# Performance work log

Hardware: AMD Instinct MI355X
Metric: run time of the kernel (lower is better)

Reference implementation:

```python
import jax, jax.numpy as jnp
import numpy as np


def setup_inputs() -> dict:
    key = jax.random.key(0)
    k1, k2, k3, k4 = jax.random.split(key, 4)
    B1, N1, B2, N2, D = 64, 128, 64, 128, 128
    v1 = jax.random.normal(k1, (B1, N1, D), dtype=jnp.float32)
    v2 = jax.random.normal(k2, (B2, N2, D), dtype=jnp.float32)
    sz1 = jax.random.randint(k3, (B1,), 0, 128, dtype=jnp.int64)
    sz2 = jax.random.randint(k4, (B2,), 0, 128, dtype=jnp.int64)
    return {"v1": v1, "sz1": sz1, "v2": v2, "sz2": sz2}


def reference(v1, sz1, v2, sz2):
    # v1: (B1, N1, D) padded node features; v2: (B2, N2, D)
    # Pairwise Euclidean distances dist[b1,b2,i,j] = ||v1[b1,i] - v2[b2,j]||
    # via the gemm identity instead of the original's 5D broadcast.
    x2 = jnp.sum(v1 * v1, axis=-1)                     # (B1, N1)
    y2 = jnp.sum(v2 * v2, axis=-1)                     # (B2, N2)
    xy = jnp.einsum('aid,bjd->abij', v1, v2)           # (B1, B2, N1, N2)
    sq = x2[:, None, :, None] + y2[None, :, None, :] - 2.0 * xy
    dist = jnp.sqrt(jnp.maximum(sq, 0.0))              # (B1, B2, N1, N2)

    N1, N2 = v1.shape[1], v2.shape[1]
    mask1 = jnp.arange(N1)[None, :] >= sz1[:, None]    # (B1, N1) padded v1 nodes
    mask2 = jnp.arange(N2)[None, :] >= sz2[:, None]    # (B2, N2) padded v2 nodes
    mask = mask1[:, None, :, None] | mask2[None, :, None, :]  # (B1, B2, N1, N2)

    # Original fills masked entries with the global max of the (unmasked) distances.
    maximum = dist.max()
    dm = jnp.where(mask, maximum, dist)

    bm1 = dm.min(axis=2)                               # min over v1 nodes -> (B1, B2, N2)
    bm2 = dm.min(axis=3)                               # min over v2 nodes -> (B1, B2, N1)
    bm1 = jnp.where(jnp.all(mask, axis=2), 0.0, bm1)   # zero fully-masked columns
    bm2 = jnp.where(jnp.all(mask, axis=3), 0.0, bm2)   # zero fully-masked rows

    return bm1.sum(axis=2) + bm2.sum(axis=2)           # (B1, B2)
```

## Files before the change

### kernel.cpp

```cpp
#include <hip/hip_runtime.h>
#include <math.h>


typedef __attribute__((ext_vector_type(8))) short short8;
typedef __attribute__((ext_vector_type(4))) float f32x4;
typedef unsigned int u32;
typedef unsigned short ushort_t;

static __device__ __forceinline__ ushort_t f32_to_bf16_rne(float f) {
    u32 b = __float_as_uint(f);
    b += 0x7FFFu + ((b >> 16) & 1u);
    return (ushort_t)(b >> 16);
}

__global__ __launch_bounds__(256) void softhd_pre(
    const float* __restrict__ v1, const float* __restrict__ v2,
    ushort_t* __restrict__ v1b, ushort_t* __restrict__ v2b,
    float* __restrict__ x2g, float* __restrict__ y2g)
{
    int flat = blockIdx.x * 256 + threadIdx.x;
    int c = flat & 15;
    int r = (flat >> 4) & 127;
    int b = (flat >> 11) & 63;
    int t = flat >> 17;

    const float* src = (t ? v2 : v1) + ((size_t)((b << 7) + r) << 7) + c * 8;
    char* dstp = (char*)((t ? v2b : v1b) + ((size_t)b << 14));

    float4 q0 = *(const float4*)(src);
    float4 q1 = *(const float4*)(src + 4);

    ushort_t h[8];
    h[0] = f32_to_bf16_rne(q0.x); h[1] = f32_to_bf16_rne(q0.y);
    h[2] = f32_to_bf16_rne(q0.z); h[3] = f32_to_bf16_rne(q0.w);
    h[4] = f32_to_bf16_rne(q1.x); h[5] = f32_to_bf16_rne(q1.y);
    h[6] = f32_to_bf16_rne(q1.z); h[7] = f32_to_bf16_rne(q1.w);

    float p = 0.f;
#pragma unroll
    for (int k = 0; k < 8; ++k) {
        float fv = __uint_as_float((u32)h[k] << 16);
        p += fv * fv;
    }

    uint4 w;
    w.x = (u32)h[0] | ((u32)h[1] << 16);
    w.y = (u32)h[2] | ((u32)h[3] << 16);
    w.z = (u32)h[4] | ((u32)h[5] << 16);
    w.w = (u32)h[6] | ((u32)h[7] << 16);

    int off = ((c >> 2) << 13) + ((r >> 3) << 9) + ((c & 3) << 7) + ((r & 7) << 4);
    *(uint4*)(dstp + off) = w;

    p += __shfl_xor(p, 1);
    p += __shfl_xor(p, 2);
    p += __shfl_xor(p, 4);
    p += __shfl_xor(p, 8);
    if (c == 0) (t ? y2g : x2g)[(b << 7) + r] = p;
}

__global__ __launch_bounds__(256, 4) void softhd_mfma(
    const ushort_t* __restrict__ v1b, const ushort_t* __restrict__ v2b,
    const float* __restrict__ x2g, const float* __restrict__ y2g,
    const int* __restrict__ sz1, const int* __restrict__ sz2,
    float* __restrict__ out)
{
    __shared__ __align__(16) ushort_t sb[2][2][4096];
    __shared__ float sx2[128], sy2[128];
    __shared__ u32 sbm1[128], sbm2[128];
    __shared__ float swsum[4];

    const int tid = threadIdx.x;
    const int lane = tid & 63;
    const int wid = tid >> 6;
    const int bid = ((blockIdx.x & 7) << 9) | (blockIdx.x >> 3);
    const int b1 = bid >> 6, b2 = bid & 63;

    const char* gp0 = (const char*)(v1b + ((size_t)b1 << 14));
    const char* gp1 = (const char*)(v2b + ((size_t)b2 << 14));

    const int n1 = min(max(sz1[b1], 0), 128);
    const int n2 = min(max(sz2[b2], 0), 128);

    if (tid < 128) {
        sx2[tid] = x2g[(b1 << 7) + tid];
        sbm1[tid] = 0x7F800000u;
    } else {
        sy2[tid - 128] = y2g[(b2 << 7) + (tid - 128)];
        sbm2[tid - 128] = 0x7F800000u;
    }
    asm volatile("" ::: "memory");

#define STAGE(d, q)                                                          \
    {                                                                        \
        _Pragma("unroll")                                                    \
        for (int e = 0; e < 2; ++e) {                                        \
            int m16 = ((e << 8) + tid) << 4;                                 \
            __builtin_amdgcn_global_load_lds(                                \
                (const __attribute__((address_space(1))) u32*)(gp0 + ((q) << 13) + m16), \
                (__attribute__((address_space(3))) u32*)((char*)&sb[d][0][0] + m16),     \
                16, 0, 0);                                                   \
            __builtin_amdgcn_global_load_lds(                                \
                (const __attribute__((address_space(1))) u32*)(gp1 + ((q) << 13) + m16), \
                (__attribute__((address_space(3))) u32*)((char*)&sb[d][1][0] + m16),     \
                16, 0, 0);                                                   \
        }                                                                    \
    }
#define WAITV4()  asm volatile("s_waitcnt vmcnt(4)" ::: "memory")
#define WAITV0()  asm volatile("s_waitcnt vmcnt(0)" ::: "memory")
#define BAR()     asm volatile("s_barrier" ::: "memory")

    STAGE(0, 0);
    STAGE(1, 1);

    const int qr = wid >> 1, qc = wid & 1;
    const int ibase = qr << 6, jbase = qc << 6;
    const int rf = lane & 15, kg = lane >> 4;

    int aoff[4], boff[4];
#pragma unroll
    for (int f = 0; f < 4; ++f) {
        int ra = ibase + (f << 4) + rf;
        int rb = jbase + (f << 4) + rf;
        aoff[f] = ((ra >> 3) << 8) + (kg << 6) + ((ra & 7) << 3);
        boff[f] = ((rb >> 3) << 8) + (kg << 6) + ((rb & 7) << 3);
    }

    f32x4 acc[4][4];
#pragma unroll
    for (int fi = 0; fi < 4; ++fi)
#pragma unroll
        for (int fj = 0; fj < 4; ++fj)
            acc[fi][fj] = (f32x4){0.f, 0.f, 0.f, 0.f};

#define COMPUTE(d)                                                           \
    {                                                                        \
        short8 a[4], b[4];                                                   \
        _Pragma("unroll")                                                    \
        for (int f = 0; f < 4; ++f) {                                        \
            a[f] = *(const short8*)(&sb[d][0][0] + aoff[f]);                 \
            b[f] = *(const short8*)(&sb[d][1][0] + boff[f]);                 \
        }                                                                    \
        _Pragma("unroll")                                                    \
        for (int fi = 0; fi < 4; ++fi)                                       \
            _Pragma("unroll")                                                \
            for (int fj = 0; fj < 4; ++fj)                                   \
                acc[fi][fj] = __builtin_amdgcn_mfma_f32_16x16x32_bf16(       \
                    a[fi], b[fj], acc[fi][fj], 0, 0, 0);                     \
    }

    WAITV4(); BAR();
    COMPUTE(0);
    BAR(); STAGE(0, 2);
    WAITV4(); BAR();
    COMPUTE(1);
    BAR(); STAGE(1, 3);
    WAITV4(); BAR();
    COMPUTE(0);
    BAR();
    WAITV0(); BAR();
    COMPUTE(1);

#undef COMPUTE
#undef STAGE
#undef WAITV4
#undef WAITV0
#undef BAR

    const float INF = __builtin_inff();

    float xie[16], yje[4];
#pragma unroll
    for (int t = 0; t < 16; ++t) {
        int i = ibase + ((t >> 2) << 4) + (kg << 2) + (t & 3);
        xie[t] = (i < n1) ? sx2[i] : INF;
    }
#pragma unroll
    for (int fj = 0; fj < 4; ++fj) {
        int j = jbase + (fj << 4) + rf;
        yje[fj] = (j < n2) ? sy2[j] : INF;
    }

    float minj[4], mini[16];
#pragma unroll
    for (int fj = 0; fj < 4; ++fj) minj[fj] = INF;
#pragma unroll
    for (int t = 0; t < 16; ++t) mini[t] = INF;

#pragma unroll
    for (int fi = 0; fi < 4; ++fi) {
        float u[4][4];
#pragma unroll
        for (int fj = 0; fj < 4; ++fj)
#pragma unroll
            for (int q = 0; q < 4; ++q)
                u[fj][q] = fmaf(acc[fi][fj][q], -2.f, xie[fi * 4 + q] + yje[fj]);
#pragma unroll
        for (int fj = 0; fj < 4; ++fj) {
            minj[fj] = fminf(fminf(minj[fj], u[fj][0]), u[fj][1]);
            minj[fj] = fminf(fminf(minj[fj], u[fj][2]), u[fj][3]);
        }
#pragma unroll
        for (int q = 0; q < 4; ++q) {
            float mt = mini[fi * 4 + q];
            mt = fminf(fminf(mt, u[0][q]), u[1][q]);
            mt = fminf(fminf(mt, u[2][q]), u[3][q]);
            mini[fi * 4 + q] = mt;
        }
    }

#pragma unroll
    for (int k = 0; k < 4; ++k) {
        const int d = 1 << k;
        const bool hi = (lane >> k) & 1;
#pragma unroll
        for (int base = 0; base < 16; base += 2 * (1 << k)) {
            float pa = fminf(mini[base], __shfl_xor(mini[base], d));
            float pb = fminf(mini[base + d], __shfl_xor(mini[base + d], d));
            mini[base] = hi ? pb : pa;
        }
    }
    {
        float dmin = __builtin_amdgcn_sqrtf(fmaxf(mini[0], 0.f));
        int i = ibase + ((rf >> 2) << 4) + (kg << 2) + (rf & 3);
        atomicMin(&sbm2[i], __float_as_uint(dmin));
    }

#pragma unroll
    for (int k = 0; k < 2; ++k) {
        const int d = 16 << k;
        const bool hi = (lane >> (4 + k)) & 1;
#pragma unroll
        for (int base = 0; base < 4; base += 2 * (1 << k)) {
            float pa = fminf(minj[base], __shfl_xor(minj[base], d));
            float pb = fminf(minj[base + (1 << k)],
                             __shfl_xor(minj[base + (1 << k)], d));
            minj[base] = hi ? pb : pa;
        }
    }
    {
        float dmin = __builtin_amdgcn_sqrtf(fmaxf(minj[0], 0.f));
        atomicMin(&sbm1[jbase + lane], __float_as_uint(dmin));
    }
    __syncthreads();

    float v = 0.f;
    if (tid < 128) {
        if (n1 > 0 && tid < n2) v += __uint_as_float(sbm1[tid]);
        if (n2 > 0 && tid < n1) v += __uint_as_float(sbm2[tid]);
    }
#pragma unroll
    for (int off = 32; off >= 1; off >>= 1) v += __shfl_down(v, off);
    if (lane == 0) swsum[wid] = v;
    __syncthreads();
    if (tid == 0) out[bid] = swsum[0] + swsum[1] + swsum[2] + swsum[3];
}

extern "C" void kernel_launch(void* const* d_in, const int* in_sizes, int n_in,
                              void* d_out, int out_size, void* d_ws, size_t ws_size,
                              hipStream_t stream) {
    const float* v1  = (const float*)d_in[0];
    const int*   sz1 = (const int*)d_in[1];
    const float* v2  = (const float*)d_in[2];
    const int*   sz2 = (const int*)d_in[3];
    float* out = (float*)d_out;
    (void)in_sizes; (void)n_in; (void)out_size; (void)ws_size;

    char* ws = (char*)d_ws;
    ushort_t* v1b = (ushort_t*)ws;
    ushort_t* v2b = (ushort_t*)(ws + (2u << 20));
    float*    x2g = (float*)(ws + (4u << 20));
    float*    y2g = x2g + 64 * 128;

    softhd_pre<<<dim3(1024), dim3(256), 0, stream>>>(v1, v2, v1b, v2b, x2g, y2g);
    softhd_mfma<<<dim3(4096), dim3(256), 0, stream>>>(v1b, v2b, x2g, y2g,
                                                      sz1, sz2, out);
}
```

Measured before the change: 36.02 us.

## Process two b2 pairs per block, prefetching second pair during first epilogue

Each block now handles one b1 against two consecutive b2 graphs, halving the grid. The second pair's first two K-stages are staged into LDS while the first pair's epilogue and reduction run, hiding load latency across the pair boundary. The epilogue is also restructured to reduce row minima per fragment with DPP swizzles instead of cross-lane shuffles, which cuts the register footprint. In exchange, each block runs a longer serialized chain and there are fewer blocks to cover tail imbalance.

```diff
diff --git a/kernel.cpp b/kernel.cpp
--- a/kernel.cpp
+++ b/kernel.cpp
@@ -12,6 +12,11 @@
     b += 0x7FFFu + ((b >> 16) & 1u);
     return (ushort_t)(b >> 16);
 }
+
+#define DPPX1(x) __int_as_float(__builtin_amdgcn_update_dpp( \
+    0, __float_as_int(x), 0xB1, 0xF, 0xF, true))
+#define DPPX2(x) __int_as_float(__builtin_amdgcn_update_dpp( \
+    0, __float_as_int(x), 0x4E, 0xF, 0xF, true))
 
 __global__ __launch_bounds__(256) void softhd_pre(
     const float* __restrict__ v1, const float* __restrict__ v2,
@@ -66,32 +71,37 @@
     float* __restrict__ out)
 {
     __shared__ __align__(16) ushort_t sb[2][2][4096];
-    __shared__ float sx2[128], sy2[128];
+    __shared__ float sx2[128], sy2[2][128];
     __shared__ u32 sbm1[128], sbm2[128];
     __shared__ float swsum[4];
 
     const int tid = threadIdx.x;
     const int lane = tid & 63;
     const int wid = tid >> 6;
-    const int bid = ((blockIdx.x & 7) << 9) | (blockIdx.x >> 3);
-    const int b1 = bid >> 6, b2 = bid & 63;
+    const int bid = ((blockIdx.x & 7) << 8) | (blockIdx.x >> 3);
+    const int b1 = bid >> 5;
+    const int b2base = (bid & 31) << 1;
 
     const char* gp0 = (const char*)(v1b + ((size_t)b1 << 14));
-    const char* gp1 = (const char*)(v2b + ((size_t)b2 << 14));
+    const char* gB0 = (const char*)(v2b + ((size_t)(b2base + 0) << 14));
+    const char* gB1 = (const char*)(v2b + ((size_t)(b2base + 1) << 14));
 
     const int n1 = min(max(sz1[b1], 0), 128);
-    const int n2 = min(max(sz2[b2], 0), 128);
+    int n2v[2];
+    n2v[0] = min(max(sz2[b2base + 0], 0), 128);
+    n2v[1] = min(max(sz2[b2base + 1], 0), 128);
 
     if (tid < 128) {
         sx2[tid] = x2g[(b1 << 7) + tid];
         sbm1[tid] = 0x7F800000u;
+        sbm2[tid] = 0x7F800000u;
     } else {
-        sy2[tid - 128] = y2g[(b2 << 7) + (tid - 128)];
-        sbm2[tid - 128] = 0x7F800000u;
+        sy2[0][tid - 128] = y2g[((b2base + 0) << 7) + (tid - 128)];
+        sy2[1][tid - 128] = y2g[((b2base + 1) << 7) + (tid - 128)];
     }
     asm volatile("" ::: "memory");
 
-#define STAGE(d, q)                                                          \
+#define STAGE(d, gB, q)                                                      \
     {                                                                        \
         _Pragma("unroll")                                                    \
         for (int e = 0; e < 2; ++e) {                                        \
@@ -101,7 +111,7 @@
                 (__attribute__((address_space(3))) u32*)((char*)&sb[d][0][0] + m16),     \
                 16, 0, 0);                                                   \
             __builtin_amdgcn_global_load_lds(                                \
-                (const __attribute__((address_space(1))) u32*)(gp1 + ((q) << 13) + m16), \
+                (const __attribute__((address_space(1))) u32*)((gB) + ((q) << 13) + m16),\
                 (__attribute__((address_space(3))) u32*)((char*)&sb[d][1][0] + m16),     \
                 16, 0, 0);                                                   \
         }                                                                    \
@@ -109,13 +119,17 @@
 #define WAITV4()  asm volatile("s_waitcnt vmcnt(4)" ::: "memory")
 #define WAITV0()  asm volatile("s_waitcnt vmcnt(0)" ::: "memory")
 #define BAR()     asm volatile("s_barrier" ::: "memory")
-
-    STAGE(0, 0);
-    STAGE(1, 1);
+#define LGKMBAR() do { asm volatile("s_waitcnt lgkmcnt(0)" ::: "memory");    \
+                       asm volatile("s_barrier" ::: "memory"); } while (0)
+
+    STAGE(0, gB0, 0);
+    STAGE(1, gB0, 1);
 
     const int qr = wid >> 1, qc = wid & 1;
     const int ibase = qr << 6, jbase = qc << 6;
     const int rf = lane & 15, kg = lane >> 4;
+    const bool h0 = lane & 1, h1 = lane & 2, h2 = lane & 4, h3 = lane & 8;
+    const bool h4 = lane & 16, h5 = lane & 32;
 
     int aoff[4], boff[4];
 #pragma unroll
@@ -149,111 +163,130 @@
                     a[fi], b[fj], acc[fi][fj], 0, 0, 0);                     \
     }
 
-    WAITV4(); BAR();
-    COMPUTE(0);
-    BAR(); STAGE(0, 2);
-    WAITV4(); BAR();
-    COMPUTE(1);
-    BAR(); STAGE(1, 3);
-    WAITV4(); BAR();
-    COMPUTE(0);
-    BAR();
-    WAITV0(); BAR();
-    COMPUTE(1);
+    const float INF = __builtin_inff();
+
+#define EPILOGUE(p)                                                          \
+    {                                                                        \
+        const int nn2 = n2v[p];                                              \
+        float yje[4];                                                        \
+        _Pragma("unroll")                                                    \
+        for (int fj = 0; fj < 4; ++fj) {                                     \
+            int j = jbase + (fj << 4) + rf;                                  \
+            yje[fj] = (j < nn2) ? sy2[p][j] : INF;                           \
+        }                                                                    \
+        float minj[4] = {INF, INF, INF, INF};                                \
+        float mini4[4];                                                      \
+        _Pragma("unroll")                                                    \
+        for (int fi = 0; fi < 4; ++fi) {                                     \
+            const int i0 = ibase + (fi << 4) + (kg << 2);                    \
+            float4 xs = *(const float4*)&sx2[i0];                            \
+            float xie[4];                                                    \
+            xie[0] = (i0 + 0 < n1) ? xs.x : INF;                             \
+            xie[1] = (i0 + 1 < n1) ? xs.y : INF;                             \
+            xie[2] = (i0 + 2 < n1) ? xs.z : INF;                             \
+            xie[3] = (i0 + 3 < n1) ? xs.w : INF;                             \
+            float u[4][4];                                                   \
+            _Pragma("unroll")                                                \
+            for (int fj = 0; fj < 4; ++fj) {                                 \
+                _Pragma("unroll")                                            \
+                for (int q = 0; q < 4; ++q)                                  \
+                    u[fj][q] = fmaf(acc[fi][fj][q], -2.f, xie[q] + yje[fj]); \
+                minj[fj] = fminf(fminf(minj[fj], u[fj][0]), u[fj][1]);       \
+                minj[fj] = fminf(fminf(minj[fj], u[fj][2]), u[fj][3]);       \
+            }                                                                \
+            float mq0 = fminf(fminf(u[0][0], u[1][0]), fminf(u[2][0], u[3][0])); \
+            float mq1 = fminf(fminf(u[0][1], u[1][1]), fminf(u[2][1], u[3][1])); \
+            float mq2 = fminf(fminf(u[0][2], u[1][2]), fminf(u[2][2], u[3][2])); \
+            float mq3 = fminf(fminf(u[0][3], u[1][3]), fminf(u[2][3], u[3][3])); \
+            float pa = fminf(mq0, DPPX1(mq0));                               \
+            float pb = fminf(mq1, DPPX1(mq1));                               \
+            float r01 = h0 ? pb : pa;                                        \
+            pa = fminf(mq2, DPPX1(mq2));                                     \
+            pb = fminf(mq3, DPPX1(mq3));                                     \
+            float r23 = h0 ? pb : pa;                                        \
+            pa = fminf(r01, DPPX2(r01));                                     \
+            pb = fminf(r23, DPPX2(r23));                                     \
+            mini4[fi] = h1 ? pb : pa;                                        \
+        }                                                                    \
+        {                                                                    \
+            float pa = fminf(mini4[0], __shfl_xor(mini4[0], 4));             \
+            float pb = fminf(mini4[1], __shfl_xor(mini4[1], 4));             \
+            float A = h2 ? pb : pa;                                          \
+            pa = fminf(mini4[2], __shfl_xor(mini4[2], 4));                   \
+            pb = fminf(mini4[3], __shfl_xor(mini4[3], 4));                   \
+            float B = h2 ? pb : pa;                                          \
+            pa = fminf(A, __shfl_xor(A, 8));                                 \
+            pb = fminf(B, __shfl_xor(B, 8));                                 \
+            float Mi = h3 ? pb : pa;                                         \
+            float dmin = __builtin_amdgcn_sqrtf(fmaxf(Mi, 0.f));             \
+            int ii = ibase + ((rf >> 2) << 4) + (kg << 2) + (rf & 3);        \
+            atomicMin(&sbm2[ii], __float_as_uint(dmin));                     \
+        }                                                                    \
+        {                                                                    \
+            float pa = fminf(minj[0], __shfl_xor(minj[0], 32));              \
+            float pb = fminf(minj[1], __shfl_xor(minj[1], 32));              \
+            float A = h5 ? pb : pa;                                          \
+            pa = fminf(minj[2], __shfl_xor(minj[2], 32));                    \
+            pb = fminf(minj[3], __shfl_xor(minj[3], 32));                    \
+            float B = h5 ? pb : pa;                                          \
+            pa = fminf(A, __shfl_xor(A, 16));                                \
+            pb = fminf(B, __shfl_xor(B, 16));                                \
+            float Mj = h4 ? pb : pa;                                         \
+            float dminj = __builtin_amdgcn_sqrtf(fmaxf(Mj, 0.f));            \
+            int fjf = ((lane >> 5) & 1) | (((lane >> 4) & 1) << 1);          \
+            atomicMin(&sbm1[jbase + (fjf << 4) + rf], __float_as_uint(dminj)); \
+        }                                                                    \
+    }
+
+#define REDUCE_OUT(p, REINIT)                                                \
+    {                                                                        \
+        LGKMBAR();                                                           \
+        const int nn2 = n2v[p];                                              \
+        float v = 0.f;                                                       \
+        if (tid < 128) {                                                     \
+            u32 m1b = sbm1[tid], m2b = sbm2[tid];                            \
+            if (n1 > 0 && tid < nn2) v += __uint_as_float(m1b);              \
+            if (nn2 > 0 && tid < n1) v += __uint_as_float(m2b);              \
+            if (REINIT) {                                                    \
+                sbm1[tid] = 0x7F800000u; sbm2[tid] = 0x7F800000u;            \
+            }                                                                \
+        }                                                                    \
+        _Pragma("unroll")                                                    \
+        for (int off = 32; off >= 1; off >>= 1) v += __shfl_down(v, off);    \
+        if (lane == 0) swsum[wid] = v;                                       \
+        LGKMBAR();                                                           \
+        if (tid == 0) out[(b1 << 6) + b2base + (p)]                          \
+            = swsum[0] + swsum[1] + swsum[2] + swsum[3];                     \
+    }
+
+    WAITV4(); BAR(); COMPUTE(0); BAR(); STAGE(0, gB0, 2);
+    WAITV4(); BAR(); COMPUTE(1); BAR(); STAGE(1, gB0, 3);
+    WAITV4(); BAR(); COMPUTE(0); BAR(); STAGE(0, gB1, 0);
+    WAITV4(); BAR(); COMPUTE(1); BAR(); STAGE(1, gB1, 1);
+    EPILOGUE(0);
+    REDUCE_OUT(0, 1);
+
+#pragma unroll
+    for (int fi = 0; fi < 4; ++fi)
+#pragma unroll
+        for (int fj = 0; fj < 4; ++fj)
+            acc[fi][fj] = (f32x4){0.f, 0.f, 0.f, 0.f};
+
+    WAITV4(); BAR(); COMPUTE(0); BAR(); STAGE(0, gB1, 2);
+    WAITV4(); BAR(); COMPUTE(1); BAR(); STAGE(1, gB1, 3);
+    WAITV4(); BAR(); COMPUTE(0); BAR();
+    WAITV0(); BAR(); COMPUTE(1);
+    EPILOGUE(1);
+    REDUCE_OUT(1, 0);
 
 #undef COMPUTE
 #undef STAGE
+#undef EPILOGUE
+#undef REDUCE_OUT
 #undef WAITV4
 #undef WAITV0
 #undef BAR
-
-    const float INF = __builtin_inff();
-
-    float xie[16], yje[4];
-#pragma unroll
-    for (int t = 0; t < 16; ++t) {
-        int i = ibase + ((t >> 2) << 4) + (kg << 2) + (t & 3);
-        xie[t] = (i < n1) ? sx2[i] : INF;
-    }
-#pragma unroll
-    for (int fj = 0; fj < 4; ++fj) {
-        int j = jbase + (fj << 4) + rf;
-        yje[fj] = (j < n2) ? sy2[j] : INF;
-    }
-
-    float minj[4], mini[16];
-#pragma unroll
-    for (int fj = 0; fj < 4; ++fj) minj[fj] = INF;
-#pragma unroll
-    for (int t = 0; t < 16; ++t) mini[t] = INF;
-
-#pragma unroll
-    for (int fi = 0; fi < 4; ++fi) {
-        float u[4][4];
-#pragma unroll
-        for (int fj = 0; fj < 4; ++fj)
-#pragma unroll
-            for (int q = 0; q < 4; ++q)
-                u[fj][q] = fmaf(acc[fi][fj][q], -2.f, xie[fi * 4 + q] + yje[fj]);
-#pragma unroll
-        for (int fj = 0; fj < 4; ++fj) {
-            minj[fj] = fminf(fminf(minj[fj], u[fj][0]), u[fj][1]);
-            minj[fj] = fminf(fminf(minj[fj], u[fj][2]), u[fj][3]);
-        }
-#pragma unroll
-        for (int q = 0; q < 4; ++q) {
-            float mt = mini[fi * 4 + q];
-            mt = fminf(fminf(mt, u[0][q]), u[1][q]);
-            mt = fminf(fminf(mt, u[2][q]), u[3][q]);
-            mini[fi * 4 + q] = mt;
-        }
-    }
-
-#pragma unroll
-    for (int k = 0; k < 4; ++k) {
-        const int d = 1 << k;
-        const bool hi = (lane >> k) & 1;
-#pragma unroll
-        for (int base = 0; base < 16; base += 2 * (1 << k)) {
-            float pa = fminf(mini[base], __shfl_xor(mini[base], d));
-            float pb = fminf(mini[base + d], __shfl_xor(mini[base + d], d));
-            mini[base] = hi ? pb : pa;
-        }
-    }
-    {
-        float dmin = __builtin_amdgcn_sqrtf(fmaxf(mini[0], 0.f));
-        int i = ibase + ((rf >> 2) << 4) + (kg << 2) + (rf & 3);
-        atomicMin(&sbm2[i], __float_as_uint(dmin));
-    }
-
-#pragma unroll
-    for (int k = 0; k < 2; ++k) {
-        const int d = 16 << k;
-        const bool hi = (lane >> (4 + k)) & 1;
-#pragma unroll
-        for (int base = 0; base < 4; base += 2 * (1 << k)) {
-            float pa = fminf(minj[base], __shfl_xor(minj[base], d));
-            float pb = fminf(minj[base + (1 << k)],
-                             __shfl_xor(minj[base + (1 << k)], d));
-            minj[base] = hi ? pb : pa;
-        }
-    }
-    {
-        float dmin = __builtin_amdgcn_sqrtf(fmaxf(minj[0], 0.f));
-        atomicMin(&sbm1[jbase + lane], __float_as_uint(dmin));
-    }
-    __syncthreads();
-
-    float v = 0.f;
-    if (tid < 128) {
-        if (n1 > 0 && tid < n2) v += __uint_as_float(sbm1[tid]);
-        if (n2 > 0 && tid < n1) v += __uint_as_float(sbm2[tid]);
-    }
-#pragma unroll
-    for (int off = 32; off >= 1; off >>= 1) v += __shfl_down(v, off);
-    if (lane == 0) swsum[wid] = v;
-    __syncthreads();
-    if (tid == 0) out[bid] = swsum[0] + swsum[1] + swsum[2] + swsum[3];
+#undef LGKMBAR
 }
 
 extern "C" void kernel_launch(void* const* d_in, const int* in_sizes, int n_in,
@@ -273,6 +306,6 @@
     float*    y2g = x2g + 64 * 128;
 
     softhd_pre<<<dim3(1024), dim3(256), 0, stream>>>(v1, v2, v1b, v2b, x2g, y2g);
-    softhd_mfma<<<dim3(4096), dim3(256), 0, stream>>>(v1b, v2b, x2g, y2g,
+    softhd_mfma<<<dim3(2048), dim3(256), 0, stream>>>(v1b, v2b, x2g, y2g,
                                                       sz1, sz2, out);
 }
```

Result: slower. 39.46 us (+9.6%).
